# Performance work log

Hardware: AMD Instinct MI355X
Metric: run time of the kernel (lower is better)

## Reference

```python
import jax, jax.numpy as jnp
import numpy as np

N, E, H, F, T = 50000, 800000, 64, 74, 4
STEPS = 4


def setup_inputs() -> dict:
    key = jax.random.key(0)
    ks = jax.random.split(key, 16)
    s = 0.05
    return {
        "x": jax.random.normal(ks[0], (N, F), jnp.float32),
        "etype": jax.random.randint(ks[1], (E,), 0, T, jnp.int32),
        "src": jax.random.randint(ks[2], (E,), 0, N, jnp.int32),
        "dst": jax.random.randint(ks[3], (E,), 0, N, jnp.int32),
        "W_in": jax.random.normal(ks[4], (F, H), jnp.float32) * s,
        "b_in": jax.random.normal(ks[5], (H,), jnp.float32) * s,
        "edge_W": jax.random.normal(ks[6], (T, H, H), jnp.float32) * s,
        "edge_b": jax.random.normal(ks[7], (T, 1), jnp.float32) * s,
        "gru_Wih": jax.random.normal(ks[8], (H, 3 * H), jnp.float32) * s,
        "gru_Whh": jax.random.normal(ks[9], (H, 3 * H), jnp.float32) * s,
        "gru_bih": jax.random.normal(ks[10], (3 * H,), jnp.float32) * s,
        "gru_bhh": jax.random.normal(ks[11], (3 * H,), jnp.float32) * s,
        "mlp_W1": jax.random.normal(ks[12], (2 * H, H), jnp.float32) * s,
        "mlp_b1": jax.random.normal(ks[13], (H,), jnp.float32) * s,
        "mlp_W2": jax.random.normal(ks[14], (H, H), jnp.float32) * s,
        "mlp_b2": jax.random.normal(ks[15], (H,), jnp.float32) * s,
    }


def _gru_cell(x, h, Wih, Whh, bih, bhh):
    gi = x @ Wih + bih  # [N, 3H]
    gh = h @ Whh + bhh
    ir, iz, inn = jnp.split(gi, 3, axis=-1)
    hr, hz, hn = jnp.split(gh, 3, axis=-1)
    r = jax.nn.sigmoid(ir + hr)
    z = jax.nn.sigmoid(iz + hz)
    n = jnp.tanh(inn + r * hn)
    return (1.0 - z) * n + z * h


def reference(x, etype, src, dst, W_in, b_in, edge_W, edge_b,
              gru_Wih, gru_Whh, gru_bih, gru_bhh,
              mlp_W1, mlp_b1, mlp_W2, mlp_b2):
    h_init = x @ W_in + b_in  # [N, H]
    h = h_init
    for _ in range(STEPS):
        # per-node transform under every edge type: [N, T, H]
        nt = jnp.einsum('ni,tio->nto', h, edge_W)
        # gather per-edge message from src node + per-type bias, ReLU
        msg = jax.nn.relu(nt[src, etype] + edge_b[etype])  # [E, H]
        agg = jax.ops.segment_sum(msg, dst, num_segments=N)  # [N, H]
        h = _gru_cell(agg, h, gru_Wih, gru_Whh, gru_bih, gru_bhh)
    cat = jnp.concatenate([h_init, h], axis=-1)  # [N, 2H]
    out = jnp.tanh(jax.nn.relu(cat @ mlp_W1 + mlp_b1) @ mlp_W2 + mlp_b2)
    return out
```

## Files before the change

kernel.cpp:

```cpp
#include <hip/hip_runtime.h>
#include <hip/hip_bf16.h>

#define N_NODES 50000
#define M2      50048
#define N_EDGES 800000
#define H 64
#define F 74
#define T 4
#define STEPS 4
#define NTILES16 (M2/16)
#define PAD_REC  (M2*4)
#define SCAN_NB  196

using short8 = __attribute__((ext_vector_type(8))) short;
using f32x4  = __attribute__((ext_vector_type(4))) float;
typedef unsigned short ushort_t;

#define MFMA(a,b,c) __builtin_amdgcn_mfma_f32_16x16x32_bf16(a,b,c,0,0,0)

static __device__ inline float b2f(ushort_t u) {
    union { unsigned int i; float f; } c; c.i = ((unsigned int)u) << 16; return c.f;
}
static __device__ inline ushort_t f2b(float v) {
    union { __hip_bfloat16 b; ushort_t u; } c; c.b = __float2bfloat16(v); return c.u;
}
static __device__ inline void split_store(ushort_t* hi, ushort_t* lo, size_t ix, float v) {
    ushort_t h = f2b(v);
    hi[ix] = h;
    lo[ix] = f2b(v - b2f(h));
}
static __device__ inline float sigm(float x) { return 1.f / (1.f + __expf(-x)); }
static __device__ inline float tanh_f(float x) {
    float e2 = __expf(2.f * x); return 1.f - 2.f / (e2 + 1.f);
}

template<int KW8>
static __device__ inline void stage_tile(const ushort_t* __restrict__ g, ushort_t* l,
                                         int rows, int tid, int nthr) {
    const int chunks = rows * KW8;
    for (int i = tid; i < chunks; i += nthr) {
        int row = i / KW8, kg = i - row * KW8;
        short8 v = *(const short8*)(g + (size_t)row * (KW8 * 8) + kg * 8);
        int b = (row * (KW8 * 16) + kg * 16) ^ ((row & 7) << 4);
        *(short8*)((char*)l + b) = v;
    }
}
template<int KW8>
static __device__ inline short8 rdfrag(const ushort_t* l, int row, int kg) {
    int b = (row * (KW8 * 16) + kg * 16) ^ ((row & 7) << 4);
    return *(const short8*)((const char*)l + b);
}
static __device__ inline short8 afrag(const ushort_t* base, int LD, int row, int kg) {
    return *(const short8*)(base + (size_t)row * LD + kg * 8);
}

__global__ __launch_bounds__(256) void split_x_kernel(
    const float* __restrict__ x, ushort_t* __restrict__ hi, ushort_t* __restrict__ lo)
{
    int idx = blockIdx.x * 256 + threadIdx.x;
    int total = M2 * 96;
    if (idx >= total) return;
    int row = idx / 96, c = idx - row * 96;
    float v = (row < N_NODES && c < F) ? x[(size_t)row * F + c] : 0.f;
    split_store(hi, lo, idx, v);
}

__global__ __launch_bounds__(256) void prep_w_kernel(
    const float* __restrict__ W_in, const float* __restrict__ eW,
    const float* __restrict__ Wih, const float* __restrict__ Whh,
    const float* __restrict__ W1, const float* __restrict__ W2,
    ushort_t* __restrict__ BtWin_hi, ushort_t* __restrict__ BtWin_lo,
    ushort_t* __restrict__ BtE_hi,
    ushort_t* __restrict__ Btg_all,
    ushort_t* __restrict__ BtW1_hi, ushort_t* __restrict__ BtW1_lo,
    ushort_t* __restrict__ BtW2_hi, ushort_t* __restrict__ BtW2_lo,
    int* __restrict__ deg, ushort_t* __restrict__ ntr_pad)
{
    int idx = blockIdx.x * 256 + threadIdx.x;
    if (idx < 6144) {
        int col = idx / 96, k = idx - col * 96;
        float v = (k < F) ? W_in[(size_t)k * 64 + col] : 0.f;
        split_store(BtWin_hi, BtWin_lo, idx, v);
    } else if (idx < 22528) {
        int i = idx - 6144;
        int c = i >> 6, k = i & 63;
        float v = eW[(c >> 6) * 4096 + k * 64 + (c & 63)];
        BtE_hi[i] = f2b(v);
    } else if (idx < 55296) {
        int i = idx - 22528;
        int hh = i >> 14;
        int r2 = i & 16383;
        int rr = r2 >> 7, k = r2 & 127;
        int g = rr >> 5, cc = rr & 31;
        int gate = (g == 3) ? 2 : g;
        int col = gate * 64 + hh * 32 + cc;
        float v = (k < 64) ? Wih[(size_t)k * 192 + col]
                           : Whh[(size_t)(k - 64) * 192 + col];
        ushort_t h = f2b(v);
        Btg_all[i] = (g == 3) ? f2b(v - b2f(h)) : h;
    } else if (idx < 63488) {
        int i = idx - 55296;
        int col = i >> 7, k = i & 127;
        float v = W1[(size_t)k * 64 + col];
        split_store(BtW1_hi, BtW1_lo, i, v);
    } else if (idx < 67584) {
        int i = idx - 63488;
        int col = i >> 6, k = i & 63;
        float v = W2[(size_t)k * 64 + col];
        split_store(BtW2_hi, BtW2_lo, i, v);
    } else if (idx < 117584) {
        deg[idx - 67584] = 0;
    } else if (idx < 117648) {
        ntr_pad[idx - 117584] = 0;
    }
}

__global__ __launch_bounds__(256) void degrank_kernel(
    const int* __restrict__ dst, int* __restrict__ deg, int* __restrict__ rank)
{
    int e = blockIdx.x * 256 + threadIdx.x;
    if (e < N_EDGES) rank[e] = atomicAdd(&deg[dst[e]], 1);
}

__global__ __launch_bounds__(256) void scan_p1(
    const int* __restrict__ deg, int* __restrict__ bsum)
{
    __shared__ int ws4[4];
    const int tid = threadIdx.x, lane = tid & 63, w = tid >> 6;
    int idx = blockIdx.x * 256 + tid;
    int v = (idx < N_NODES) ? deg[idx] : 0;
#pragma unroll
    for (int off = 32; off >= 1; off >>= 1) v += __shfl_down(v, off, 64);
    if (lane == 0) ws4[w] = v;
    __syncthreads();
    if (tid == 0) bsum[blockIdx.x] = ws4[0] + ws4[1] + ws4[2] + ws4[3];
}

__global__ __launch_bounds__(256) void scan_p2(
    const int* __restrict__ bsum, int* __restrict__ boff, int* __restrict__ rowp)
{
    __shared__ int ws4[4];
    const int tid = threadIdx.x, lane = tid & 63, w = tid >> 6;
    int v = (tid < SCAN_NB) ? bsum[tid] : 0;
    int x = v;
#pragma unroll
    for (int off = 1; off < 64; off <<= 1) {
        int u = __shfl_up(x, off, 64);
        if (lane >= off) x += u;
    }
    if (lane == 63) ws4[w] = x;
    __syncthreads();
    int a0 = ws4[0], a1 = ws4[1], a2 = ws4[2];
    int add = (w > 0 ? a0 : 0) + (w > 1 ? a1 : 0) + (w > 2 ? a2 : 0);
    if (tid < SCAN_NB) boff[tid] = add + x - v;
    if (tid == 255) rowp[N_NODES] = add + x;
}

__global__ __launch_bounds__(256) void scan_p3(
    const int* __restrict__ deg, const int* __restrict__ boff,
    int* __restrict__ rowp)
{
    __shared__ int ws4[4];
    const int tid = threadIdx.x, lane = tid & 63, w = tid >> 6;
    int idx = blockIdx.x * 256 + tid;
    int v = (idx < N_NODES) ? deg[idx] : 0;
    int x = v;
#pragma unroll
    for (int off = 1; off < 64; off <<= 1) {
        int u = __shfl_up(x, off, 64);
        if (lane >= off) x += u;
    }
    if (lane == 63) ws4[w] = x;
    __syncthreads();
    int a0 = ws4[0], a1 = ws4[1], a2 = ws4[2];
    int add = boff[blockIdx.x]
            + (w > 0 ? a0 : 0) + (w > 1 ? a1 : 0) + (w > 2 ? a2 : 0);
    if (idx < N_NODES) rowp[idx] = add + x - v;
}

__global__ __launch_bounds__(256) void fill2_kernel(
    const int* __restrict__ src, const int* __restrict__ etype,
    const int* __restrict__ dst, const int* __restrict__ rowp,
    const int* __restrict__ rank, int* __restrict__ ss)
{
    int e = blockIdx.x * 256 + threadIdx.x;
    if (e < N_EDGES)
        ss[rowp[dst[e]] + rank[e]] = src[e] * 4 + etype[e];
}

__global__ __launch_bounds__(256) void init_gemm(
    const ushort_t* __restrict__ xhi, const ushort_t* __restrict__ xlo,
    const ushort_t* __restrict__ Bh, const ushort_t* __restrict__ Bl,
    const float* __restrict__ b_in,
    ushort_t* __restrict__ cat_hi, ushort_t* __restrict__ cat_lo,
    ushort_t* __restrict__ hin_hi, ushort_t* __restrict__ hin_lo)
{
    __shared__ ushort_t lds[12288];
    ushort_t* LBh = lds;
    ushort_t* LBl = lds + 6144;
    const int tid = threadIdx.x, lane = tid & 63, wid = tid >> 6;
    const int lr = lane & 15, g = lane >> 4;
    stage_tile<12>(Bh, LBh, 64, tid, 256);
    stage_tile<12>(Bl, LBl, 64, tid, 256);
    __syncthreads();
    for (int wt = blockIdx.x * 4 + wid; wt < NTILES16; wt += gridDim.x * 4) {
        const ushort_t* pAh = xhi + (size_t)wt * 16 * 96;
        const ushort_t* pAl = xlo + (size_t)wt * 16 * 96;
        f32x4 acc[4];
        f32x4 zz = {0.f, 0.f, 0.f, 0.f};
#pragma unroll
        for (int f = 0; f < 4; ++f) acc[f] = zz;
#pragma unroll
        for (int ks = 0; ks < 3; ++ks) {
            int kg = ks * 4 + g;
            short8 ah = afrag(pAh, 96, lr, kg);
            short8 al = afrag(pAl, 96, lr, kg);
#pragma unroll
            for (int f = 0; f < 4; ++f) {
                short8 bh = rdfrag<12>(LBh, f * 16 + lr, kg);
                short8 bl = rdfrag<12>(LBl, f * 16 + lr, kg);
                acc[f] = MFMA(ah, bh, acc[f]);
                acc[f] = MFMA(ah, bl, acc[f]);
                acc[f] = MFMA(al, bh, acc[f]);
            }
        }
#pragma unroll
        for (int f = 0; f < 4; ++f) {
            int o = lr + f * 16;
            float b = b_in[o];
#pragma unroll
            for (int q = 0; q < 4; ++q) {
                int m = wt * 16 + g * 4 + q;
                if (m < N_NODES) {
                    float v = acc[f][q] + b;
                    split_store(cat_hi, cat_lo, (size_t)m * 128 + 64 + o, v);
                    split_store(hin_hi, hin_lo, (size_t)m * 64 + o, v);
                }
            }
        }
    }
}

__global__ __launch_bounds__(512, 2) void nt_gemm(
    const ushort_t* __restrict__ ahi,
    const ushort_t* __restrict__ Bh,
    const float* __restrict__ edge_b, ushort_t* __restrict__ ntr)
{
    __shared__ ushort_t lds[16384];
    const int tid = threadIdx.x, lane = tid & 63, wid = tid >> 6;
    const int lr = lane & 15, g = lane >> 4;
    stage_tile<8>(Bh, lds, 256, tid, 512);
    __syncthreads();
    for (int wt = blockIdx.x * 8 + wid; wt < NTILES16; wt += gridDim.x * 8) {
        const ushort_t* pA = ahi + (size_t)wt * 16 * 128;
        f32x4 acc[16];
        f32x4 zz = {0.f, 0.f, 0.f, 0.f};
#pragma unroll
        for (int f = 0; f < 16; ++f) acc[f] = zz;
#pragma unroll
        for (int ks = 0; ks < 2; ++ks) {
            int kg = ks * 4 + g;
            short8 ah = afrag(pA, 128, lr, kg);
#pragma unroll
            for (int f = 0; f < 16; ++f) {
                short8 bh = rdfrag<8>(lds, f * 16 + lr, kg);
                acc[f] = MFMA(ah, bh, acc[f]);
            }
        }
#pragma unroll
        for (int f = 0; f < 16; ++f) {
            int colg = lr + f * 16;
            float b = edge_b[colg >> 6];
#pragma unroll
            for (int q = 0; q < 4; ++q) {
                int m = wt * 16 + g * 4 + q;
                if (m < N_NODES) {
                    float v = fmaxf(acc[f][q] + b, 0.f);
                    ntr[(size_t)m * 256 + colg] = f2b(v);
                }
            }
        }
    }
}

__global__ __launch_bounds__(256, 4) void agg_kernel(
    const ushort_t* __restrict__ ntr, const int* __restrict__ row_ptr,
    const int* __restrict__ ss, ushort_t* __restrict__ cat_hi,
    ushort_t* __restrict__ cat_lo)
{
    const int lane = threadIdx.x & 63;
    const int w = __builtin_amdgcn_readfirstlane((int)(threadIdx.x >> 6));
    const int d = blockIdx.x * 4 + w;
    if (d >= N_NODES) return;
    const int beg = row_ptr[d];
    const int end = row_ptr[d + 1];
    float acc = 0.f;
    for (int p = beg; p < end; p += 16) {
        float v[16];
#pragma unroll
        for (int i = 0; i < 16; ++i) {
            bool inb = (p + i) < end;
            int rec = ss[inb ? (p + i) : beg];
            rec = inb ? rec : PAD_REC;
            v[i] = b2f(ntr[(size_t)rec * 64 + lane]);
        }
        float s0 = (v[0] + v[1]) + (v[2] + v[3]);
        float s1 = (v[4] + v[5]) + (v[6] + v[7]);
        float s2 = (v[8] + v[9]) + (v[10] + v[11]);
        float s3 = (v[12] + v[13]) + (v[14] + v[15]);
        acc += (s0 + s1) + (s2 + s3);
    }
    split_store(cat_hi, cat_lo, (size_t)d * 128 + lane, acc);
}

__global__ __launch_bounds__(512, 2) void gru3_gemm(
    const ushort_t* __restrict__ catXhi, const ushort_t* __restrict__ catXlo,
    const ushort_t* __restrict__ Btg,
    const float* __restrict__ bih, const float* __restrict__ bhh,
    ushort_t* __restrict__ catYhi, ushort_t* __restrict__ catYlo)
{
    __shared__ ushort_t lds[32768];
    const int tid = threadIdx.x, lane = tid & 63, wid = tid >> 6;
    const int lr = lane & 15, g = lane >> 4;
    stage_tile<16>(Btg, lds, 256, tid, 512);
    __syncthreads();
    const int hh = wid >> 2;
    const int ooff = hh * 32;
    const int bb = hh * 128;
    for (int wt0 = blockIdx.x * 4; wt0 < NTILES16; wt0 += gridDim.x * 4) {
        const int wt = wt0 + (wid & 3);
        const ushort_t* pAh = catXhi + (size_t)wt * 16 * 128;
        const ushort_t* pAl = catXlo + (size_t)wt * 16 * 128;
        f32x4 aR[2], aZ[2], aIN[2], aHN[2];
        f32x4 zz = {0.f, 0.f, 0.f, 0.f};
#pragma unroll
        for (int f = 0; f < 2; ++f) { aR[f] = zz; aZ[f] = zz; aIN[f] = zz; aHN[f] = zz; }
#pragma unroll
        for (int ks = 0; ks < 4; ++ks) {
            int kg = ks * 4 + g;
            short8 ah = afrag(pAh, 128, lr, kg);
            short8 al = afrag(pAl, 128, lr, kg);
#pragma unroll
            for (int f = 0; f < 2; ++f) {
                short8 bhr = rdfrag<16>(lds, bb + f * 16 + lr, kg);
                aR[f] = MFMA(ah, bhr, aR[f]);
                aR[f] = MFMA(al, bhr, aR[f]);
                short8 bhz = rdfrag<16>(lds, bb + 32 + f * 16 + lr, kg);
                aZ[f] = MFMA(ah, bhz, aZ[f]);
                aZ[f] = MFMA(al, bhz, aZ[f]);
                short8 bhn = rdfrag<16>(lds, bb + 64 + f * 16 + lr, kg);
                short8 bln = rdfrag<16>(lds, bb + 96 + f * 16 + lr, kg);
                if (ks < 2) {
                    aIN[f] = MFMA(ah, bhn, aIN[f]);
                    aIN[f] = MFMA(al, bhn, aIN[f]);
                    aIN[f] = MFMA(ah, bln, aIN[f]);
                } else {
                    aHN[f] = MFMA(ah, bhn, aHN[f]);
                    aHN[f] = MFMA(al, bhn, aHN[f]);
                    aHN[f] = MFMA(ah, bln, aHN[f]);
                }
            }
        }
#pragma unroll
        for (int f = 0; f < 2; ++f) {
            int o = ooff + f * 16 + lr;
            float br = bih[o] + bhh[o];
            float bz = bih[64 + o] + bhh[64 + o];
            float bi_n = bih[128 + o];
            float bh_n = bhh[128 + o];
#pragma unroll
            for (int q = 0; q < 4; ++q) {
                int m = wt * 16 + g * 4 + q;
                if (m < N_NODES) {
                    float r = sigm(aR[f][q] + br);
                    float z = sigm(aZ[f][q] + bz);
                    float inn = aIN[f][q] + bi_n;
                    float hn = aHN[f][q] + bh_n;
                    float nn = tanh_f(inn + r * hn);
                    size_t hix = (size_t)m * 128 + 64 + o;
                    float hp = b2f(catXhi[hix]) + b2f(catXlo[hix]);
                    float hv = (1.f - z) * nn + z * hp;
                    split_store(catYhi, catYlo, hix, hv);
                }
            }
        }
    }
}

__global__ __launch_bounds__(256) void mlp_fused(
    const ushort_t* __restrict__ hin_hi, const ushort_t* __restrict__ hin_lo,
    const ushort_t* __restrict__ cathi, const ushort_t* __restrict__ catlo,
    const ushort_t* __restrict__ B1h, const ushort_t* __restrict__ B1l,
    const float* __restrict__ b1,
    const ushort_t* __restrict__ B2h, const ushort_t* __restrict__ B2l,
    const float* __restrict__ b2, float* __restrict__ out)
{
    __shared__ ushort_t l1h[8192];
    __shared__ ushort_t l1l[8192];
    __shared__ ushort_t l2h[4096];
    __shared__ ushort_t l2l[4096];
    __shared__ ushort_t th[4][1024];
    __shared__ ushort_t tl[4][1024];
    const int tid = threadIdx.x, lane = tid & 63, wid = tid >> 6;
    const int lr = lane & 15, g = lane >> 4;
    stage_tile<16>(B1h, l1h, 64, tid, 256);
    stage_tile<16>(B1l, l1l, 64, tid, 256);
    stage_tile<8>(B2h, l2h, 64, tid, 256);
    stage_tile<8>(B2l, l2l, 64, tid, 256);
    __syncthreads();
    char* myh = (char*)th[wid];
    char* myl = (char*)tl[wid];
    for (int wt = blockIdx.x * 4 + wid; wt < NTILES16; wt += gridDim.x * 4) {
        const ushort_t* pAh0 = hin_hi + (size_t)wt * 16 * 64;
        const ushort_t* pAl0 = hin_lo + (size_t)wt * 16 * 64;
        const ushort_t* pAh1 = cathi + (size_t)wt * 16 * 128;
        const ushort_t* pAl1 = catlo + (size_t)wt * 16 * 128;
        f32x4 acc[4];
        f32x4 zz = {0.f, 0.f, 0.f, 0.f};
#pragma unroll
        for (int f = 0; f < 4; ++f) acc[f] = zz;
#pragma unroll
        for (int ks = 0; ks < 4; ++ks) {
            int kg = ks * 4 + g;
            short8 ah, al;
            if (ks < 2) {
                ah = afrag(pAh0, 64, lr, kg);
                al = afrag(pAl0, 64, lr, kg);
            } else {
                ah = afrag(pAh1, 128, lr, (ks - 2) * 4 + g);
                al = afrag(pAl1, 128, lr, (ks - 2) * 4 + g);
            }
#pragma unroll
            for (int f = 0; f < 4; ++f) {
                short8 bh = rdfrag<16>(l1h, f * 16 + lr, kg);
                short8 bl = rdfrag<16>(l1l, f * 16 + lr, kg);
                acc[f] = MFMA(ah, bh, acc[f]);
                acc[f] = MFMA(ah, bl, acc[f]);
                acc[f] = MFMA(al, bh, acc[f]);
            }
        }
#pragma unroll
        for (int f = 0; f < 4; ++f) {
            int col = f * 16 + lr;
            float b = b1[col];
#pragma unroll
            for (int q = 0; q < 4; ++q) {
                int row = g * 4 + q;
                float v = fmaxf(acc[f][q] + b, 0.f);
                int byt = (row * 128 + col * 2) ^ ((row & 7) << 4);
                ushort_t hv = f2b(v);
                *(ushort_t*)(myh + byt) = hv;
                *(ushort_t*)(myl + byt) = f2b(v - b2f(hv));
            }
        }
        f32x4 acc2[4];
#pragma unroll
        for (int f = 0; f < 4; ++f) acc2[f] = zz;
#pragma unroll
        for (int ks = 0; ks < 2; ++ks) {
            int kg = ks * 4 + g;
            int byt = (lr * 128 + kg * 16) ^ ((lr & 7) << 4);
            short8 ah = *(const short8*)(myh + byt);
            short8 al = *(const short8*)(myl + byt);
#pragma unroll
            for (int f = 0; f < 4; ++f) {
                short8 bh = rdfrag<8>(l2h, f * 16 + lr, kg);
                short8 bl = rdfrag<8>(l2l, f * 16 + lr, kg);
                acc2[f] = MFMA(ah, bh, acc2[f]);
                acc2[f] = MFMA(ah, bl, acc2[f]);
                acc2[f] = MFMA(al, bh, acc2[f]);
            }
        }
#pragma unroll
        for (int f = 0; f < 4; ++f) {
            int o = lr + f * 16;
            float b = b2[o];
#pragma unroll
            for (int q = 0; q < 4; ++q) {
                int m = wt * 16 + g * 4 + q;
                if (m < N_NODES)
                    out[(size_t)m * 64 + o] = tanh_f(acc2[f][q] + b);
            }
        }
    }
}

extern "C" void kernel_launch(void* const* d_in, const int* in_sizes, int n_in,
                              void* d_out, int out_size, void* d_ws, size_t ws_size,
                              hipStream_t stream)
{
    const float* x      = (const float*)d_in[0];
    const int*   etype  = (const int*)  d_in[1];
    const int*   src    = (const int*)  d_in[2];
    const int*   dst    = (const int*)  d_in[3];
    const float* W_in   = (const float*)d_in[4];
    const float* b_in   = (const float*)d_in[5];
    const float* edge_W = (const float*)d_in[6];
    const float* edge_b = (const float*)d_in[7];
    const float* gWih   = (const float*)d_in[8];
    const float* gWhh   = (const float*)d_in[9];
    const float* gbih   = (const float*)d_in[10];
    const float* gbhh   = (const float*)d_in[11];
    const float* W1     = (const float*)d_in[12];
    const float* b1     = (const float*)d_in[13];
    const float* W2     = (const float*)d_in[14];
    const float* b2     = (const float*)d_in[15];
    float* out = (float*)d_out;

    char* ws = (char*)d_ws;
    ushort_t* ntr     = (ushort_t*)(ws);
    ushort_t* x_hi    = (ushort_t*)(ws);
    ushort_t* x_lo    = (ushort_t*)(ws + 9609216);
    int*      rank    = (int*)     (ws + 19660800);
    ushort_t* catA_hi = (ushort_t*)(ws + 25625088);
    ushort_t* catA_lo = (ushort_t*)(ws + 38437376);
    ushort_t* catB_hi = (ushort_t*)(ws + 51249664);
    ushort_t* catB_lo = (ushort_t*)(ws + 64061952);
    ushort_t* hin_hi  = (ushort_t*)(ws + 76874240);
    ushort_t* hin_lo  = (ushort_t*)(ws + 83280384);
    char* wbase = ws + 89686528;
    ushort_t* BtWin_hi = (ushort_t*)(wbase);
    ushort_t* BtWin_lo = (ushort_t*)(wbase + 12288);
    ushort_t* BtE_hi   = (ushort_t*)(wbase + 24576);
    ushort_t* Btg_all  = (ushort_t*)(wbase + 57344);
    ushort_t* BtW1_hi  = (ushort_t*)(wbase + 122880);
    ushort_t* BtW1_lo  = (ushort_t*)(wbase + 139264);
    ushort_t* BtW2_hi  = (ushort_t*)(wbase + 155648);
    ushort_t* BtW2_lo  = (ushort_t*)(wbase + 163840);
    char* cbase = ws + 89891328;
    int* deg    = (int*)(cbase);
    int* rowp   = (int*)(cbase + 200192);
    int* ss     = (int*)(cbase + 400640);
    int* bsum   = (int*)(cbase + 3600640);
    int* boff   = (int*)(cbase + 3601664);

    const int edge_tblocks = (N_EDGES + 255) / 256;
    const int agg_blocks = (N_NODES + 3) / 4;
    const int GB  = 782;
    const int GB8 = 512;
    const int GBF = 512;

    prep_w_kernel<<<(117648 + 255) / 256, 256, 0, stream>>>(
        W_in, edge_W, gWih, gWhh, W1, W2,
        BtWin_hi, BtWin_lo, BtE_hi, Btg_all,
        BtW1_hi, BtW1_lo, BtW2_hi, BtW2_lo,
        deg, ntr + (size_t)M2 * 256);
    split_x_kernel<<<(M2 * 96 + 255) / 256, 256, 0, stream>>>(x, x_hi, x_lo);

    degrank_kernel<<<edge_tblocks, 256, 0, stream>>>(dst, deg, rank);
    scan_p1<<<SCAN_NB, 256, 0, stream>>>(deg, bsum);
    scan_p2<<<1, 256, 0, stream>>>(bsum, boff, rowp);
    scan_p3<<<SCAN_NB, 256, 0, stream>>>(deg, boff, rowp);
    fill2_kernel<<<edge_tblocks, 256, 0, stream>>>(src, etype, dst, rowp, rank, ss);

    init_gemm<<<GB, 256, 0, stream>>>(x_hi, x_lo, BtWin_hi, BtWin_lo, b_in,
                                      catA_hi, catA_lo, hin_hi, hin_lo);

    ushort_t *Xhi = catA_hi, *Xlo = catA_lo, *Yhi = catB_hi, *Ylo = catB_lo;
    for (int s = 0; s < STEPS; ++s) {
        nt_gemm<<<GB8, 512, 0, stream>>>(Xhi + 64, BtE_hi, edge_b, ntr);
        agg_kernel<<<agg_blocks, 256, 0, stream>>>(ntr, rowp, ss, Xhi, Xlo);
        gru3_gemm<<<GBF, 512, 0, stream>>>(Xhi, Xlo, Btg_all, gbih, gbhh,
                                           Yhi, Ylo);
        ushort_t* t;
        t = Xhi; Xhi = Yhi; Yhi = t;
        t = Xlo; Xlo = Ylo; Ylo = t;
    }

    mlp_fused<<<GB, 256, 0, stream>>>(hin_hi, hin_lo, Xhi + 64, Xlo + 64,
                                      BtW1_hi, BtW1_lo, b1,
                                      BtW2_hi, BtW2_lo, b2, out);
}
```

Measured before the change: 366.0 us.

## Fuse segment-sum aggregation into GRU GEMM and drop concatenated state layout

```diff
diff --git a/kernel.cpp b/kernel.cpp
--- a/kernel.cpp
+++ b/kernel.cpp
@@ -54,27 +54,18 @@
     return *(const short8*)(base + (size_t)row * LD + kg * 8);
 }
 
-__global__ __launch_bounds__(256) void split_x_kernel(
-    const float* __restrict__ x, ushort_t* __restrict__ hi, ushort_t* __restrict__ lo)
-{
-    int idx = blockIdx.x * 256 + threadIdx.x;
-    int total = M2 * 96;
-    if (idx >= total) return;
-    int row = idx / 96, c = idx - row * 96;
-    float v = (row < N_NODES && c < F) ? x[(size_t)row * F + c] : 0.f;
-    split_store(hi, lo, idx, v);
-}
-
 __global__ __launch_bounds__(256) void prep_w_kernel(
     const float* __restrict__ W_in, const float* __restrict__ eW,
     const float* __restrict__ Wih, const float* __restrict__ Whh,
     const float* __restrict__ W1, const float* __restrict__ W2,
+    const float* __restrict__ x,
     ushort_t* __restrict__ BtWin_hi, ushort_t* __restrict__ BtWin_lo,
     ushort_t* __restrict__ BtE_hi,
-    ushort_t* __restrict__ Btg_all,
+    ushort_t* __restrict__ BtgHi, ushort_t* __restrict__ BtgLo,
     ushort_t* __restrict__ BtW1_hi, ushort_t* __restrict__ BtW1_lo,
     ushort_t* __restrict__ BtW2_hi, ushort_t* __restrict__ BtW2_lo,
-    int* __restrict__ deg, ushort_t* __restrict__ ntr_pad)
+    int* __restrict__ deg, ushort_t* __restrict__ ntr_pad,
+    ushort_t* __restrict__ x_hi, ushort_t* __restrict__ x_lo)
 {
     int idx = blockIdx.x * 256 + threadIdx.x;
     if (idx < 6144) {
@@ -86,18 +77,26 @@
         int c = i >> 6, k = i & 63;
         float v = eW[(c >> 6) * 4096 + k * 64 + (c & 63)];
         BtE_hi[i] = f2b(v);
+    } else if (idx < 47104) {
+        int i = idx - 22528;
+        int hh = i / 12288;
+        int r2 = i - hh * 12288;
+        int rr = r2 >> 7, k = r2 & 127;
+        int gg = rr >> 5, cc = rr & 31;
+        int col = gg * 64 + hh * 32 + cc;
+        float v = (k < 64) ? Wih[(size_t)k * 192 + col]
+                           : Whh[(size_t)(k - 64) * 192 + col];
+        BtgHi[i] = f2b(v);
     } else if (idx < 55296) {
-        int i = idx - 22528;
-        int hh = i >> 14;
-        int r2 = i & 16383;
-        int rr = r2 >> 7, k = r2 & 127;
-        int g = rr >> 5, cc = rr & 31;
-        int gate = (g == 3) ? 2 : g;
-        int col = gate * 64 + hh * 32 + cc;
+        int i = idx - 47104;
+        int hh = i >> 12;
+        int r2 = i & 4095;
+        int cc = r2 >> 7, k = r2 & 127;
+        int col = 128 + hh * 32 + cc;
         float v = (k < 64) ? Wih[(size_t)k * 192 + col]
                            : Whh[(size_t)(k - 64) * 192 + col];
         ushort_t h = f2b(v);
-        Btg_all[i] = (g == 3) ? f2b(v - b2f(h)) : h;
+        BtgLo[i] = f2b(v - b2f(h));
     } else if (idx < 63488) {
         int i = idx - 55296;
         int col = i >> 7, k = i & 127;
@@ -112,6 +111,13 @@
         deg[idx - 67584] = 0;
     } else if (idx < 117648) {
         ntr_pad[idx - 117584] = 0;
+    } else {
+        int i = idx - 117648;
+        if (i < M2 * 96) {
+            int row = i / 96, c = i - row * 96;
+            float v = (row < N_NODES && c < F) ? x[(size_t)row * F + c] : 0.f;
+            split_store(x_hi, x_lo, i, v);
+        }
     }
 }
 
@@ -192,7 +198,7 @@
     const ushort_t* __restrict__ xhi, const ushort_t* __restrict__ xlo,
     const ushort_t* __restrict__ Bh, const ushort_t* __restrict__ Bl,
     const float* __restrict__ b_in,
-    ushort_t* __restrict__ cat_hi, ushort_t* __restrict__ cat_lo,
+    ushort_t* __restrict__ h_hi, ushort_t* __restrict__ h_lo,
     ushort_t* __restrict__ hin_hi, ushort_t* __restrict__ hin_lo)
 {
     __shared__ ushort_t lds[12288];
@@ -233,7 +239,7 @@
                 int m = wt * 16 + g * 4 + q;
                 if (m < N_NODES) {
                     float v = acc[f][q] + b;
-                    split_store(cat_hi, cat_lo, (size_t)m * 128 + 64 + o, v);
+                    split_store(h_hi, h_lo, (size_t)m * 64 + o, v);
                     split_store(hin_hi, hin_lo, (size_t)m * 64 + o, v);
                 }
             }
@@ -242,7 +248,7 @@
 }
 
 __global__ __launch_bounds__(512, 2) void nt_gemm(
-    const ushort_t* __restrict__ ahi,
+    const ushort_t* __restrict__ hhi,
     const ushort_t* __restrict__ Bh,
     const float* __restrict__ edge_b, ushort_t* __restrict__ ntr)
 {
@@ -252,7 +258,7 @@
     stage_tile<8>(Bh, lds, 256, tid, 512);
     __syncthreads();
     for (int wt = blockIdx.x * 8 + wid; wt < NTILES16; wt += gridDim.x * 8) {
-        const ushort_t* pA = ahi + (size_t)wt * 16 * 128;
+        const ushort_t* pA = hhi + (size_t)wt * 16 * 64;
         f32x4 acc[16];
         f32x4 zz = {0.f, 0.f, 0.f, 0.f};
 #pragma unroll
@@ -260,7 +266,7 @@
 #pragma unroll
         for (int ks = 0; ks < 2; ++ks) {
             int kg = ks * 4 + g;
-            short8 ah = afrag(pA, 128, lr, kg);
+            short8 ah = afrag(pA, 64, lr, kg);
 #pragma unroll
             for (int f = 0; f < 16; ++f) {
                 short8 bh = rdfrag<8>(lds, f * 16 + lr, kg);
@@ -283,105 +289,118 @@
     }
 }
 
-__global__ __launch_bounds__(256, 4) void agg_kernel(
-    const ushort_t* __restrict__ ntr, const int* __restrict__ row_ptr,
-    const int* __restrict__ ss, ushort_t* __restrict__ cat_hi,
-    ushort_t* __restrict__ cat_lo)
-{
-    const int lane = threadIdx.x & 63;
-    const int w = __builtin_amdgcn_readfirstlane((int)(threadIdx.x >> 6));
-    const int d = blockIdx.x * 4 + w;
-    if (d >= N_NODES) return;
-    const int beg = row_ptr[d];
-    const int end = row_ptr[d + 1];
-    float acc = 0.f;
-    for (int p = beg; p < end; p += 16) {
-        float v[16];
-#pragma unroll
-        for (int i = 0; i < 16; ++i) {
-            bool inb = (p + i) < end;
-            int rec = ss[inb ? (p + i) : beg];
-            rec = inb ? rec : PAD_REC;
-            v[i] = b2f(ntr[(size_t)rec * 64 + lane]);
-        }
-        float s0 = (v[0] + v[1]) + (v[2] + v[3]);
-        float s1 = (v[4] + v[5]) + (v[6] + v[7]);
-        float s2 = (v[8] + v[9]) + (v[10] + v[11]);
-        float s3 = (v[12] + v[13]) + (v[14] + v[15]);
-        acc += (s0 + s1) + (s2 + s3);
-    }
-    split_store(cat_hi, cat_lo, (size_t)d * 128 + lane, acc);
-}
-
-__global__ __launch_bounds__(512, 2) void gru3_gemm(
-    const ushort_t* __restrict__ catXhi, const ushort_t* __restrict__ catXlo,
-    const ushort_t* __restrict__ Btg,
+__global__ __launch_bounds__(512, 2) void aggru_gemm(
+    const ushort_t* __restrict__ ntr, const int* __restrict__ rowp,
+    const int* __restrict__ ss,
+    const ushort_t* __restrict__ Xhi, const ushort_t* __restrict__ Xlo,
+    const ushort_t* __restrict__ BtgHi,
+    const ushort_t* __restrict__ BtgLo,
     const float* __restrict__ bih, const float* __restrict__ bhh,
-    ushort_t* __restrict__ catYhi, ushort_t* __restrict__ catYlo)
-{
-    __shared__ ushort_t lds[32768];
+    ushort_t* __restrict__ Yhi, ushort_t* __restrict__ Ylo)
+{
+    __shared__ ushort_t ldsB[24576];
+    __shared__ ushort_t aggh[4096];
+    __shared__ ushort_t aggl[4096];
     const int tid = threadIdx.x, lane = tid & 63, wid = tid >> 6;
     const int lr = lane & 15, g = lane >> 4;
-    stage_tile<16>(Btg, lds, 256, tid, 512);
-    __syncthreads();
-    const int hh = wid >> 2;
+    stage_tile<16>(BtgHi, ldsB, 192, tid, 512);
+
+    const int base = blockIdx.x * 64;
+#pragma unroll 1
+    for (int j = 0; j < 8; ++j) {
+        int r = wid * 8 + j;
+        int d = base + r;
+        float acc = 0.f;
+        if (d < N_NODES) {
+            const int beg = rowp[d];
+            const int end = rowp[d + 1];
+            for (int p = beg; p < end; p += 16) {
+                float v[16];
+#pragma unroll
+                for (int i = 0; i < 16; ++i) {
+                    bool inb = (p + i) < end;
+                    int rec = ss[inb ? (p + i) : beg];
+                    rec = inb ? rec : PAD_REC;
+                    v[i] = b2f(ntr[(size_t)rec * 64 + lane]);
+                }
+                float s0 = (v[0] + v[1]) + (v[2] + v[3]);
+                float s1 = (v[4] + v[5]) + (v[6] + v[7]);
+                float s2 = (v[8] + v[9]) + (v[10] + v[11]);
+                float s3 = (v[12] + v[13]) + (v[14] + v[15]);
+                acc += (s0 + s1) + (s2 + s3);
+            }
+        }
+        int byt = (r * 128 + lane * 2) ^ ((r & 7) << 4);
+        ushort_t hv = f2b(acc);
+        *(ushort_t*)((char*)aggh + byt) = hv;
+        *(ushort_t*)((char*)aggl + byt) = f2b(acc - b2f(hv));
+    }
+    __syncthreads();
+
+    const int rt = wid & 3, hh = wid >> 2;
     const int ooff = hh * 32;
-    const int bb = hh * 128;
-    for (int wt0 = blockIdx.x * 4; wt0 < NTILES16; wt0 += gridDim.x * 4) {
-        const int wt = wt0 + (wid & 3);
-        const ushort_t* pAh = catXhi + (size_t)wt * 16 * 128;
-        const ushort_t* pAl = catXlo + (size_t)wt * 16 * 128;
-        f32x4 aR[2], aZ[2], aIN[2], aHN[2];
-        f32x4 zz = {0.f, 0.f, 0.f, 0.f};
-#pragma unroll
-        for (int f = 0; f < 2; ++f) { aR[f] = zz; aZ[f] = zz; aIN[f] = zz; aHN[f] = zz; }
-#pragma unroll
-        for (int ks = 0; ks < 4; ++ks) {
-            int kg = ks * 4 + g;
-            short8 ah = afrag(pAh, 128, lr, kg);
-            short8 al = afrag(pAl, 128, lr, kg);
-#pragma unroll
-            for (int f = 0; f < 2; ++f) {
-                short8 bhr = rdfrag<16>(lds, bb + f * 16 + lr, kg);
-                aR[f] = MFMA(ah, bhr, aR[f]);
-                aR[f] = MFMA(al, bhr, aR[f]);
-                short8 bhz = rdfrag<16>(lds, bb + 32 + f * 16 + lr, kg);
-                aZ[f] = MFMA(ah, bhz, aZ[f]);
-                aZ[f] = MFMA(al, bhz, aZ[f]);
-                short8 bhn = rdfrag<16>(lds, bb + 64 + f * 16 + lr, kg);
-                short8 bln = rdfrag<16>(lds, bb + 96 + f * 16 + lr, kg);
-                if (ks < 2) {
-                    aIN[f] = MFMA(ah, bhn, aIN[f]);
-                    aIN[f] = MFMA(al, bhn, aIN[f]);
-                    aIN[f] = MFMA(ah, bln, aIN[f]);
-                } else {
-                    aHN[f] = MFMA(ah, bhn, aHN[f]);
-                    aHN[f] = MFMA(al, bhn, aHN[f]);
-                    aHN[f] = MFMA(ah, bln, aHN[f]);
-                }
-            }
+    const int bb = hh * 96;
+    const int wt = blockIdx.x * 4 + rt;
+    const ushort_t* pXh = Xhi + (size_t)wt * 16 * 64;
+    const ushort_t* pXl = Xlo + (size_t)wt * 16 * 64;
+    const ushort_t* pBln = BtgLo + (size_t)hh * 32 * 128;
+    f32x4 aR[2], aZ[2], aIN[2], aHN[2];
+    f32x4 zz = {0.f, 0.f, 0.f, 0.f};
+#pragma unroll
+    for (int f = 0; f < 2; ++f) { aR[f] = zz; aZ[f] = zz; aIN[f] = zz; aHN[f] = zz; }
+#pragma unroll
+    for (int ks = 0; ks < 4; ++ks) {
+        int kg = ks * 4 + g;
+        short8 ah, al;
+        if (ks < 2) {
+            int arow = rt * 16 + lr;
+            ah = rdfrag<8>(aggh, arow, kg);
+            al = rdfrag<8>(aggl, arow, kg);
+        } else {
+            ah = afrag(pXh, 64, lr, kg - 8);
+            al = afrag(pXl, 64, lr, kg - 8);
         }
 #pragma unroll
         for (int f = 0; f < 2; ++f) {
-            int o = ooff + f * 16 + lr;
-            float br = bih[o] + bhh[o];
-            float bz = bih[64 + o] + bhh[64 + o];
-            float bi_n = bih[128 + o];
-            float bh_n = bhh[128 + o];
-#pragma unroll
-            for (int q = 0; q < 4; ++q) {
-                int m = wt * 16 + g * 4 + q;
-                if (m < N_NODES) {
-                    float r = sigm(aR[f][q] + br);
-                    float z = sigm(aZ[f][q] + bz);
-                    float inn = aIN[f][q] + bi_n;
-                    float hn = aHN[f][q] + bh_n;
-                    float nn = tanh_f(inn + r * hn);
-                    size_t hix = (size_t)m * 128 + 64 + o;
-                    float hp = b2f(catXhi[hix]) + b2f(catXlo[hix]);
-                    float hv = (1.f - z) * nn + z * hp;
-                    split_store(catYhi, catYlo, hix, hv);
-                }
+            short8 bhr = rdfrag<16>(ldsB, bb + f * 16 + lr, kg);
+            aR[f] = MFMA(ah, bhr, aR[f]);
+            aR[f] = MFMA(al, bhr, aR[f]);
+            short8 bhz = rdfrag<16>(ldsB, bb + 32 + f * 16 + lr, kg);
+            aZ[f] = MFMA(ah, bhz, aZ[f]);
+            aZ[f] = MFMA(al, bhz, aZ[f]);
+            short8 bhn = rdfrag<16>(ldsB, bb + 64 + f * 16 + lr, kg);
+            short8 bln = afrag(pBln, 128, f * 16 + lr, kg);
+            if (ks < 2) {
+                aIN[f] = MFMA(ah, bhn, aIN[f]);
+                aIN[f] = MFMA(al, bhn, aIN[f]);
+                aIN[f] = MFMA(ah, bln, aIN[f]);
+            } else {
+                aHN[f] = MFMA(ah, bhn, aHN[f]);
+                aHN[f] = MFMA(al, bhn, aHN[f]);
+                aHN[f] = MFMA(ah, bln, aHN[f]);
+            }
+        }
+    }
+#pragma unroll
+    for (int f = 0; f < 2; ++f) {
+        int o = ooff + f * 16 + lr;
+        float br = bih[o] + bhh[o];
+        float bz = bih[64 + o] + bhh[64 + o];
+        float bi_n = bih[128 + o];
+        float bh_n = bhh[128 + o];
+#pragma unroll
+        for (int q = 0; q < 4; ++q) {
+            int m = wt * 16 + g * 4 + q;
+            if (m < N_NODES) {
+                float r = sigm(aR[f][q] + br);
+                float z = sigm(aZ[f][q] + bz);
+                float inn = aIN[f][q] + bi_n;
+                float hn = aHN[f][q] + bh_n;
+                float nn = tanh_f(inn + r * hn);
+                size_t hix = (size_t)m * 64 + o;
+                float hp = b2f(Xhi[hix]) + b2f(Xlo[hix]);
+                float hv = (1.f - z) * nn + z * hp;
+                split_store(Yhi, Ylo, hix, hv);
             }
         }
     }
@@ -389,7 +408,7 @@
 
 __global__ __launch_bounds__(256) void mlp_fused(
     const ushort_t* __restrict__ hin_hi, const ushort_t* __restrict__ hin_lo,
-    const ushort_t* __restrict__ cathi, const ushort_t* __restrict__ catlo,
+    const ushort_t* __restrict__ hhi, const ushort_t* __restrict__ hlo,
     const ushort_t* __restrict__ B1h, const ushort_t* __restrict__ B1l,
     const float* __restrict__ b1,
     const ushort_t* __restrict__ B2h, const ushort_t* __restrict__ B2l,
@@ -413,8 +432,8 @@
     for (int wt = blockIdx.x * 4 + wid; wt < NTILES16; wt += gridDim.x * 4) {
         const ushort_t* pAh0 = hin_hi + (size_t)wt * 16 * 64;
         const ushort_t* pAl0 = hin_lo + (size_t)wt * 16 * 64;
-        const ushort_t* pAh1 = cathi + (size_t)wt * 16 * 128;
-        const ushort_t* pAl1 = catlo + (size_t)wt * 16 * 128;
+        const ushort_t* pAh1 = hhi + (size_t)wt * 16 * 64;
+        const ushort_t* pAl1 = hlo + (size_t)wt * 16 * 64;
         f32x4 acc[4];
         f32x4 zz = {0.f, 0.f, 0.f, 0.f};
 #pragma unroll
@@ -427,8 +446,8 @@
                 ah = afrag(pAh0, 64, lr, kg);
                 al = afrag(pAl0, 64, lr, kg);
             } else {
-                ah = afrag(pAh1, 128, lr, (ks - 2) * 4 + g);
-                al = afrag(pAl1, 128, lr, (ks - 2) * 4 + g);
+                ah = afrag(pAh1, 64, lr, kg - 8);
+                al = afrag(pAl1, 64, lr, kg - 8);
             }
 #pragma unroll
             for (int f = 0; f < 4; ++f) {
@@ -508,26 +527,27 @@
     float* out = (float*)d_out;
 
     char* ws = (char*)d_ws;
-    ushort_t* ntr     = (ushort_t*)(ws);
-    ushort_t* x_hi    = (ushort_t*)(ws);
-    ushort_t* x_lo    = (ushort_t*)(ws + 9609216);
-    int*      rank    = (int*)     (ws + 19660800);
-    ushort_t* catA_hi = (ushort_t*)(ws + 25625088);
-    ushort_t* catA_lo = (ushort_t*)(ws + 38437376);
-    ushort_t* catB_hi = (ushort_t*)(ws + 51249664);
-    ushort_t* catB_lo = (ushort_t*)(ws + 64061952);
-    ushort_t* hin_hi  = (ushort_t*)(ws + 76874240);
-    ushort_t* hin_lo  = (ushort_t*)(ws + 83280384);
-    char* wbase = ws + 89686528;
+    ushort_t* ntr    = (ushort_t*)(ws);
+    ushort_t* x_hi   = (ushort_t*)(ws);
+    ushort_t* x_lo   = (ushort_t*)(ws + 9609216);
+    int*      rank   = (int*)     (ws + 19660800);
+    ushort_t* hA_hi  = (ushort_t*)(ws + 25625088);
+    ushort_t* hA_lo  = (ushort_t*)(ws + 32031232);
+    ushort_t* hB_hi  = (ushort_t*)(ws + 38437376);
+    ushort_t* hB_lo  = (ushort_t*)(ws + 44843520);
+    ushort_t* hin_hi = (ushort_t*)(ws + 51249664);
+    ushort_t* hin_lo = (ushort_t*)(ws + 57655808);
+    char* wbase = ws + 64061952;
     ushort_t* BtWin_hi = (ushort_t*)(wbase);
     ushort_t* BtWin_lo = (ushort_t*)(wbase + 12288);
     ushort_t* BtE_hi   = (ushort_t*)(wbase + 24576);
-    ushort_t* Btg_all  = (ushort_t*)(wbase + 57344);
+    ushort_t* BtgHi    = (ushort_t*)(wbase + 57344);
+    ushort_t* BtgLo    = (ushort_t*)(wbase + 106496);
     ushort_t* BtW1_hi  = (ushort_t*)(wbase + 122880);
     ushort_t* BtW1_lo  = (ushort_t*)(wbase + 139264);
     ushort_t* BtW2_hi  = (ushort_t*)(wbase + 155648);
     ushort_t* BtW2_lo  = (ushort_t*)(wbase + 163840);
-    char* cbase = ws + 89891328;
+    char* cbase = ws + 64233984;
     int* deg    = (int*)(cbase);
     int* rowp   = (int*)(cbase + 200192);
     int* ss     = (int*)(cbase + 400640);
@@ -535,17 +555,16 @@
     int* boff   = (int*)(cbase + 3601664);
 
     const int edge_tblocks = (N_EDGES + 255) / 256;
-    const int agg_blocks = (N_NODES + 3) / 4;
     const int GB  = 782;
     const int GB8 = 512;
-    const int GBF = 512;
-
-    prep_w_kernel<<<(117648 + 255) / 256, 256, 0, stream>>>(
-        W_in, edge_W, gWih, gWhh, W1, W2,
-        BtWin_hi, BtWin_lo, BtE_hi, Btg_all,
+    ushort_t* ntr_pad = ntr + (size_t)M2 * 256;
+
+    const int PREP_TOTAL = 117648 + M2 * 96;
+    prep_w_kernel<<<(PREP_TOTAL + 255) / 256, 256, 0, stream>>>(
+        W_in, edge_W, gWih, gWhh, W1, W2, x,
+        BtWin_hi, BtWin_lo, BtE_hi, BtgHi, BtgLo,
         BtW1_hi, BtW1_lo, BtW2_hi, BtW2_lo,
-        deg, ntr + (size_t)M2 * 256);
-    split_x_kernel<<<(M2 * 96 + 255) / 256, 256, 0, stream>>>(x, x_hi, x_lo);
+        deg, ntr_pad, x_hi, x_lo);
 
     degrank_kernel<<<edge_tblocks, 256, 0, stream>>>(dst, deg, rank);
     scan_p1<<<SCAN_NB, 256, 0, stream>>>(deg, bsum);
@@ -554,20 +573,19 @@
     fill2_kernel<<<edge_tblocks, 256, 0, stream>>>(src, etype, dst, rowp, rank, ss);
 
     init_gemm<<<GB, 256, 0, stream>>>(x_hi, x_lo, BtWin_hi, BtWin_lo, b_in,
-                                      catA_hi, catA_lo, hin_hi, hin_lo);
-
-    ushort_t *Xhi = catA_hi, *Xlo = catA_lo, *Yhi = catB_hi, *Ylo = catB_lo;
+                                      hA_hi, hA_lo, hin_hi, hin_lo);
+
+    ushort_t *Xhi = hA_hi, *Xlo = hA_lo, *Yhi = hB_hi, *Ylo = hB_lo;
     for (int s = 0; s < STEPS; ++s) {
-        nt_gemm<<<GB8, 512, 0, stream>>>(Xhi + 64, BtE_hi, edge_b, ntr);
-        agg_kernel<<<agg_blocks, 256, 0, stream>>>(ntr, rowp, ss, Xhi, Xlo);
-        gru3_gemm<<<GBF, 512, 0, stream>>>(Xhi, Xlo, Btg_all, gbih, gbhh,
-                                           Yhi, Ylo);
+        nt_gemm<<<GB8, 512, 0, stream>>>(Xhi, BtE_hi, edge_b, ntr);
+        aggru_gemm<<<GB, 512, 0, stream>>>(ntr, rowp, ss, Xhi, Xlo,
+                                           BtgHi, BtgLo, gbih, gbhh, Yhi, Ylo);
         ushort_t* t;
         t = Xhi; Xhi = Yhi; Yhi = t;
         t = Xlo; Xlo = Ylo; Ylo = t;
     }
 
-    mlp_fused<<<GB, 256, 0, stream>>>(hin_hi, hin_lo, Xhi + 64, Xlo + 64,
+    mlp_fused<<<GB, 256, 0, stream>>>(hin_hi, hin_lo, Xhi, Xlo,
                                       BtW1_hi, BtW1_lo, b1,
                                       BtW2_hi, BtW2_lo, b2, out);
 }
```

Result: slower. 402.3 us (+9.9%).
